# Performance work log

Hardware: AMD Instinct MI355X
Metric: run time of the kernel (lower is better)

## Reference

```python
import jax, jax.numpy as jnp
import numpy as np

# --- module hyperparameters (init_kwargs) ---
K = 64
PZ, PY, PX = 5, 5, 5          # patch_size
PROJ = 512                     # projection_dim
B, C, D, H, W = 4, 256, 32, 64, 64


def setup_inputs() -> dict:
    key = jax.random.key(0)
    k1, k2, k3, k4 = jax.random.split(key, 4)
    feature_map = jax.random.normal(k1, (B, C, D, H, W), jnp.float32)
    score_map = jax.random.normal(k2, (B, 1, D, H, W), jnp.float32)
    # LazyLinear(projection_dim) materialized: in_features = C * K
    Wp = jax.random.normal(k3, (PROJ, C * K), jnp.float32) / np.sqrt(C * K).astype(np.float32)
    b = jax.random.normal(k4, (PROJ,), jnp.float32) * 0.01
    return {"feature_map": feature_map, "score_map": score_map, "Wp": Wp, "b": b}


def reference(feature_map, score_map, Wp, b):
    Bn, Cn, Dn, Hn, Wn = feature_map.shape
    flat = score_map.reshape(Bn, -1)                      # (B, D*H*W)
    scores, idx = jax.lax.top_k(flat, K)                  # (B, K)
    z = idx // (Hn * Wn)
    y = (idx % (Hn * Wn)) // Wn
    x = idx % Wn
    centers = jnp.stack([z, y, x], axis=-1)               # (B, K, 3)

    # boundary-clamped window origins: z0 = max(cz - dz//2, 0), window [z0, min(z0+dz, D))
    z0 = jnp.maximum(z - PZ // 2, 0)
    y0 = jnp.maximum(y - PY // 2, 0)
    x0 = jnp.maximum(x - PX // 2, 0)

    def per_batch(fm, z0b, y0b, x0b):
        # fm: (C, D, H, W); z0b/y0b/x0b: (K,)
        iz = z0b[:, None] + jnp.arange(PZ)                # (K, PZ)
        iy = y0b[:, None] + jnp.arange(PY)
        ix = x0b[:, None] + jnp.arange(PX)
        mz, my, mx = iz < Dn, iy < Hn, ix < Wn            # out-of-range => excluded from mean
        iz = jnp.minimum(iz, Dn - 1)
        iy = jnp.minimum(iy, Hn - 1)
        ix = jnp.minimum(ix, Wn - 1)
        # gather fixed-size patches: (C, K, PZ, PY, PX)
        patch = fm[:, iz[:, :, None, None], iy[:, None, :, None], ix[:, None, None, :]]
        mask = (mz[:, :, None, None] & my[:, None, :, None] & mx[:, None, None, :]).astype(fm.dtype)  # (K,PZ,PY,PX)
        s = jnp.einsum('ckzyx,kzyx->kc', patch, mask)     # masked sum -> (K, C)
        cnt = mask.sum(axis=(-3, -2, -1))                 # (K,) = actual clamped patch volume
        return (s / cnt[:, None]).reshape(-1)             # (K*C,) — patch-major, matching torch cat order

    vec = jax.vmap(per_batch)(feature_map, z0, y0, x0)    # (B, K*C)
    feature = vec @ Wp.T + b                              # (B, PROJ)
    return centers, scores, feature
```

## Files before the change

### kernel.cpp

```cpp
#include <hip/hip_runtime.h>
#include <hip/hip_bf16.h>

#define Bn   4
#define Cn   256
#define Dn   32
#define Hn   64
#define Wn   64
#define Kt   64
#define PROJ 512
#define DHW  (Dn*Hn*Wn)
#define HW   (Hn*Wn)
#define VECLEN (Kt*Cn)

#define NBIN    4096
#define CANDMAX 4096
#define STATIC_THR 3.0f

#define WS_CNT_OFF  0
#define WS_IDX_OFF  1024
#define WS_CAND_OFF 4096
#define WS_VEC_OFF  (256*1024)

#define OUT_SCORES 768
#define OUT_FEAT   1024

__device__ __forceinline__ unsigned f2sortable(float f) {
    unsigned u = __float_as_uint(f);
    return (u & 0x80000000u) ? ~u : (u | 0x80000000u);
}
__device__ __forceinline__ float sortable2f(unsigned u) {
    unsigned orig = (u & 0x80000000u) ? (u & 0x7FFFFFFFu) : ~u;
    return __uint_as_float(orig);
}

__global__ __launch_bounds__(256) void compact_kernel(
        const float* __restrict__ score, unsigned long long* __restrict__ cand,
        int* __restrict__ cnt) {
    const int blk = blockIdx.x;
    const int b   = blk >> 6;
    const int sub = blk & 63;
    const int tid = threadIdx.x;
    const unsigned thr = f2sortable(STATIC_THR);

    const float4* src = (const float4*)(score + (size_t)b * DHW) + sub * 512;
    unsigned long long* cb = cand + (size_t)b * CANDMAX;
    #pragma unroll
    for (int i = tid; i < 512; i += 256) {
        float4 v = src[i];
        unsigned gbase = (unsigned)((sub * 512 + i) * 4);
        float vals[4] = {v.x, v.y, v.z, v.w};
        #pragma unroll
        for (int l = 0; l < 4; ++l) {
            unsigned u = f2sortable(vals[l]);
            if (u >= thr) {
                int pos = atomicAdd(&cnt[b], 1);
                if (pos < CANDMAX)
                    cb[pos] = ((unsigned long long)u << 32) |
                              (0xFFFFFFFFu - (gbase + l));
            }
        }
    }
}

__global__ __launch_bounds__(512) void final_kernel(
        const float* __restrict__ score,
        const unsigned long long* __restrict__ cand, const int* __restrict__ cnt,
        float* __restrict__ out, int* __restrict__ topk_idx) {
    __shared__ unsigned long long keys[CANDMAX];
    __shared__ int lh[NBIN];
    __shared__ int partial[256];
    __shared__ int s_cnt, s_thr;
    const int b   = blockIdx.x;
    const int tid = threadIdx.x;

    int n = cnt[b];
    if (n >= Kt && n <= CANDMAX) {
        const unsigned long long* cb = cand + (size_t)b * CANDMAX;
        for (int i = tid; i < n; i += 512) keys[i] = cb[i];
    } else {
        for (int i = tid; i < NBIN; i += 512) lh[i] = 0;
        if (tid == 0) s_cnt = 0;
        __syncthreads();
        const float4* src = (const float4*)(score + (size_t)b * DHW);
        for (int i = tid; i < DHW / 4; i += 512) {
            float4 v = src[i];
            atomicAdd(&lh[f2sortable(v.x) >> 20], 1);
            atomicAdd(&lh[f2sortable(v.y) >> 20], 1);
            atomicAdd(&lh[f2sortable(v.z) >> 20], 1);
            atomicAdd(&lh[f2sortable(v.w) >> 20], 1);
        }
        __syncthreads();
        if (tid < 256) {
            int base = NBIN - 16 - 16 * tid;
            int s = 0;
            #pragma unroll
            for (int i = 0; i < 16; ++i) s += lh[base + i];
            partial[tid] = s;
        }
        __syncthreads();
        if (tid == 0) {
            int cum = 0, T = 0;
            for (int j = 0; j < 256; ++j) {
                if (cum + partial[j] >= Kt) {
                    int bb = NBIN - 1 - 16 * j;
                    for (int i = 0; i < 16; ++i) {
                        cum += lh[bb - i];
                        if (cum >= Kt) { T = bb - i; break; }
                    }
                    break;
                }
                cum += partial[j];
            }
            s_thr = T;
        }
        __syncthreads();
        const unsigned thr = (unsigned)s_thr;
        for (int i = tid; i < DHW / 4; i += 512) {
            float4 v = src[i];
            float vals[4] = {v.x, v.y, v.z, v.w};
            #pragma unroll
            for (int l = 0; l < 4; ++l) {
                unsigned u = f2sortable(vals[l]);
                if ((u >> 20) >= thr) {
                    int pos = atomicAdd(&s_cnt, 1);
                    if (pos < CANDMAX)
                        keys[pos] = ((unsigned long long)u << 32) |
                                    (0xFFFFFFFFu - (unsigned)(4 * i + l));
                }
            }
        }
        __syncthreads();
        n = s_cnt;
        if (n > CANDMAX) n = CANDMAX;
    }

    int P = 64;
    while (P < n) P <<= 1;
    for (int i = tid; i < P; i += 512)
        if (i >= n) keys[i] = 0ULL;
    __syncthreads();

    for (int k = 2; k <= P; k <<= 1) {
        for (int j = k >> 1; j > 0; j >>= 1) {
            for (int i = tid; i < P; i += 512) {
                int ixj = i ^ j;
                if (ixj > i) {
                    unsigned long long a = keys[i], c = keys[ixj];
                    bool desc = ((i & k) == 0);
                    if (desc ? (a < c) : (a > c)) { keys[i] = c; keys[ixj] = a; }
                }
            }
            __syncthreads();
        }
    }

    if (tid < Kt) {
        unsigned long long kk = keys[tid];
        float sc = sortable2f((unsigned)(kk >> 32));
        unsigned gidx = 0xFFFFFFFFu - (unsigned)(kk & 0xFFFFFFFFu);
        int z = (int)(gidx >> 12);
        int y = (int)((gidx >> 6) & 63);
        int x = (int)(gidx & 63);
        int o = (b * Kt + tid) * 3;
        out[o + 0] = (float)z;
        out[o + 1] = (float)y;
        out[o + 2] = (float)x;
        out[OUT_SCORES + b * Kt + tid] = sc;
        topk_idx[b * Kt + tid] = (int)gidx;
    }
}

__global__ __launch_bounds__(256) void gather_kernel(
        const float* __restrict__ fm, const int* __restrict__ topk_idx,
        float* __restrict__ vec) {
    const int blk = blockIdx.x;
    const int b   = blk >> 6;
    const int cg  = blk & 63;
    const int tid = threadIdx.x;
    const int k   = tid & 63;
    const int c   = cg * 4 + (tid >> 6);

    const int idx = topk_idx[b * Kt + k];
    const int z = idx >> 12;
    const int y = (idx >> 6) & 63;
    const int x = idx & 63;
    const int z0 = max(z - 2, 0), y0 = max(y - 2, 0), x0 = max(x - 2, 0);
    const int nz = min(5, Dn - z0), ny = min(5, Hn - y0), nx = min(5, Wn - x0);
    const int xe = x0 + nx;
    const int a0 = x0 & ~3;
    const bool need2 = (a0 + 4) < xe;

    float m[8];
    #pragma unroll
    for (int j = 0; j < 8; ++j) {
        int e = a0 + j;
        m[j] = (e >= x0 && e < xe) ? 1.f : 0.f;
    }

    const float* base = fm + ((size_t)(b * Cn + c)) * DHW
                           + (size_t)z0 * HW + (size_t)y0 * Wn;
    float s = 0.f;
    #pragma unroll
    for (int iz = 0; iz < 5; ++iz) {
        #pragma unroll
        for (int iy = 0; iy < 5; ++iy) {
            if (iz < nz && iy < ny) {
                const float* row = base + iz * HW + iy * Wn;
                float4 v0 = *(const float4*)(row + a0);
                s = fmaf(v0.x, m[0], s);
                s = fmaf(v0.y, m[1], s);
                s = fmaf(v0.z, m[2], s);
                s = fmaf(v0.w, m[3], s);
                if (need2) {
                    float4 v1 = *(const float4*)(row + a0 + 4);
                    s = fmaf(v1.x, m[4], s);
                    s = fmaf(v1.y, m[5], s);
                    s = fmaf(v1.z, m[6], s);
                    s = fmaf(v1.w, m[7], s);
                }
            }
        }
    }
    vec[((size_t)(b * Kt + k) << 8) + c] = s / (float)(nz * ny * nx);
}

__global__ __launch_bounds__(256) void gemv_kernel(
        const float* __restrict__ vec, const float* __restrict__ Wp,
        const float* __restrict__ bias, float* __restrict__ out) {
    const int p   = blockIdx.x;
    const int tid = threadIdx.x;
    const float4* w4 = (const float4*)(Wp + (size_t)p * VECLEN);

    float acc[Bn] = {0.f, 0.f, 0.f, 0.f};
    for (int i = tid; i < VECLEN / 4; i += 256) {
        float4 wv = w4[i];
        #pragma unroll
        for (int bb = 0; bb < Bn; ++bb) {
            float4 vv = ((const float4*)(vec + bb * VECLEN))[i];
            acc[bb] += wv.x * vv.x + wv.y * vv.y + wv.z * vv.z + wv.w * vv.w;
        }
    }

    __shared__ float red[4][Bn];
    const int lane = tid & 63, wave = tid >> 6;
    #pragma unroll
    for (int bb = 0; bb < Bn; ++bb) {
        float v = acc[bb];
        #pragma unroll
        for (int off = 32; off > 0; off >>= 1) v += __shfl_down(v, off, 64);
        if (lane == 0) red[wave][bb] = v;
    }
    __syncthreads();
    if (tid < Bn) {
        int bb = tid;
        float t = red[0][bb] + red[1][bb] + red[2][bb] + red[3][bb];
        out[OUT_FEAT + bb * PROJ + p] = t + bias[p];
    }
}

extern "C" void kernel_launch(void* const* d_in, const int* in_sizes, int n_in,
                              void* d_out, int out_size, void* d_ws, size_t ws_size,
                              hipStream_t stream) {
    const float* fm    = (const float*)d_in[0];
    const float* score = (const float*)d_in[1];
    const float* Wp    = (const float*)d_in[2];
    const float* bias  = (const float*)d_in[3];
    float* out = (float*)d_out;

    char* ws = (char*)d_ws;
    int*   cand_cnt = (int*)(ws + WS_CNT_OFF);
    int*   topk_idx = (int*)(ws + WS_IDX_OFF);
    unsigned long long* cand = (unsigned long long*)(ws + WS_CAND_OFF);
    float* vec      = (float*)(ws + WS_VEC_OFF);

    hipMemsetAsync(cand_cnt, 0, Bn * sizeof(int), stream);
    compact_kernel<<<Bn * 64, 256, 0, stream>>>(score, cand, cand_cnt);
    final_kernel<<<Bn, 512, 0, stream>>>(score, cand, cand_cnt, out, topk_idx);
    gather_kernel<<<Bn * 64, 256, 0, stream>>>(fm, topk_idx, vec);
    gemv_kernel<<<PROJ, 256, 0, stream>>>(vec, Wp, bias, out);
}
```

Before: 71.00 us.

## Use per-block candidate slots and rank-based top-k selection instead of bitonic sort

Compaction now gathers candidates in shared memory per block and writes them to a fixed per-block slot with a count header. This removes the global atomics and the memset launch. The final kernel prefix-sums the slot counts, gathers the keys, and picks the top-K by counting ranks with an O(n^2) comparison instead of a full bitonic sort, now using 256 threads. The risk is the quadratic rank cost if the candidate count is large, plus a fallback path whenever any slot overflows.

```diff
diff --git a/kernel.cpp b/kernel.cpp
--- a/kernel.cpp
+++ b/kernel.cpp
@@ -14,12 +14,12 @@
 
 #define NBIN    4096
 #define CANDMAX 4096
+#define SLOT    128
 #define STATIC_THR 3.0f
 
-#define WS_CNT_OFF  0
-#define WS_IDX_OFF  1024
-#define WS_CAND_OFF 4096
-#define WS_VEC_OFF  (256*1024)
+#define WS_CAND_OFF 0
+#define WS_IDX_OFF  (256*1024)
+#define WS_VEC_OFF  (260*1024)
 
 #define OUT_SCORES 768
 #define OUT_FEAT   1024
@@ -34,16 +34,18 @@
 }
 
 __global__ __launch_bounds__(256) void compact_kernel(
-        const float* __restrict__ score, unsigned long long* __restrict__ cand,
-        int* __restrict__ cnt) {
+        const float* __restrict__ score, unsigned long long* __restrict__ cand) {
+    __shared__ unsigned long long lc[SLOT - 1];
+    __shared__ int lcnt;
     const int blk = blockIdx.x;
     const int b   = blk >> 6;
     const int sub = blk & 63;
     const int tid = threadIdx.x;
+    if (tid == 0) lcnt = 0;
+    __syncthreads();
+
     const unsigned thr = f2sortable(STATIC_THR);
-
     const float4* src = (const float4*)(score + (size_t)b * DHW) + sub * 512;
-    unsigned long long* cb = cand + (size_t)b * CANDMAX;
     #pragma unroll
     for (int i = tid; i < 512; i += 256) {
         float4 v = src[i];
@@ -53,36 +55,65 @@
         for (int l = 0; l < 4; ++l) {
             unsigned u = f2sortable(vals[l]);
             if (u >= thr) {
-                int pos = atomicAdd(&cnt[b], 1);
-                if (pos < CANDMAX)
-                    cb[pos] = ((unsigned long long)u << 32) |
+                int pos = atomicAdd(&lcnt, 1);
+                if (pos < SLOT - 1)
+                    lc[pos] = ((unsigned long long)u << 32) |
                               (0xFFFFFFFFu - (gbase + l));
             }
         }
     }
-}
-
-__global__ __launch_bounds__(512) void final_kernel(
+    __syncthreads();
+
+    unsigned long long* cb = cand + (size_t)blk * SLOT;
+    int n = lcnt;
+    if (n > SLOT - 1) n = SLOT;
+    if (tid == 0) cb[0] = (unsigned long long)n;
+    int m = (n > SLOT - 1) ? (SLOT - 1) : n;
+    for (int i = tid; i < m; i += 256) cb[1 + i] = lc[i];
+}
+
+__global__ __launch_bounds__(256) void final_kernel(
         const float* __restrict__ score,
-        const unsigned long long* __restrict__ cand, const int* __restrict__ cnt,
+        const unsigned long long* __restrict__ cand,
         float* __restrict__ out, int* __restrict__ topk_idx) {
     __shared__ unsigned long long keys[CANDMAX];
+    __shared__ unsigned long long win[Kt];
     __shared__ int lh[NBIN];
     __shared__ int partial[256];
-    __shared__ int s_cnt, s_thr;
+    __shared__ int cnts[64], offs[64];
+    __shared__ int s_n, s_thr, s_cnt, s_ovf;
     const int b   = blockIdx.x;
     const int tid = threadIdx.x;
 
-    int n = cnt[b];
-    if (n >= Kt && n <= CANDMAX) {
-        const unsigned long long* cb = cand + (size_t)b * CANDMAX;
-        for (int i = tid; i < n; i += 512) keys[i] = cb[i];
+    if (tid == 0) { s_ovf = 0; s_cnt = 0; }
+    __syncthreads();
+    if (tid < 64) {
+        int c = (int)cand[(size_t)((b << 6) + tid) * SLOT];
+        if (c > SLOT - 1) atomicOr(&s_ovf, 1);
+        cnts[tid] = c;
+    }
+    __syncthreads();
+    if (tid == 0) {
+        int o = 0;
+        for (int s = 0; s < 64; ++s) { offs[s] = o; o += cnts[s]; }
+        s_n = o;
+    }
+    __syncthreads();
+
+    int n = s_n;
+    if (!s_ovf && n >= Kt && n <= CANDMAX) {
+        for (int s = 0; s < 64; ++s) {
+            int c = cnts[s], o = offs[s];
+            const unsigned long long* cb =
+                cand + (size_t)((b << 6) + s) * SLOT + 1;
+            for (int i = tid; i < c; i += 256) keys[o + i] = cb[i];
+        }
+        __syncthreads();
     } else {
-        for (int i = tid; i < NBIN; i += 512) lh[i] = 0;
-        if (tid == 0) s_cnt = 0;
+        for (int i = tid; i < NBIN; i += 256) lh[i] = 0;
         __syncthreads();
         const float4* src = (const float4*)(score + (size_t)b * DHW);
-        for (int i = tid; i < DHW / 4; i += 512) {
+        for (int i = tid; i < DHW / 4; i += 256) {
             float4 v = src[i];
             atomicAdd(&lh[f2sortable(v.x) >> 20], 1);
             atomicAdd(&lh[f2sortable(v.y) >> 20], 1);
@@ -90,7 +121,7 @@
             atomicAdd(&lh[f2sortable(v.w) >> 20], 1);
         }
         __syncthreads();
-        if (tid < 256) {
+        {
             int base = NBIN - 16 - 16 * tid;
             int s = 0;
             #pragma unroll
@@ -115,7 +146,7 @@
         }
         __syncthreads();
         const unsigned thr = (unsigned)s_thr;
-        for (int i = tid; i < DHW / 4; i += 512) {
+        for (int i = tid; i < DHW / 4; i += 256) {
             float4 v = src[i];
             float vals[4] = {v.x, v.y, v.z, v.w};
             #pragma unroll
@@ -134,28 +165,16 @@
         if (n > CANDMAX) n = CANDMAX;
     }
 
-    int P = 64;
-    while (P < n) P <<= 1;
-    for (int i = tid; i < P; i += 512)
-        if (i >= n) keys[i] = 0ULL;
-    __syncthreads();
-
-    for (int k = 2; k <= P; k <<= 1) {
-        for (int j = k >> 1; j > 0; j >>= 1) {
-            for (int i = tid; i < P; i += 512) {
-                int ixj = i ^ j;
-                if (ixj > i) {
-                    unsigned long long a = keys[i], c = keys[ixj];
-                    bool desc = ((i & k) == 0);
-                    if (desc ? (a < c) : (a > c)) { keys[i] = c; keys[ixj] = a; }
-                }
-            }
-            __syncthreads();
-        }
-    }
+    for (int i = tid; i < n; i += 256) {
+        unsigned long long k = keys[i];
+        int r = 0;
+        for (int j = 0; j < n; ++j) r += (keys[j] > k);
+        if (r < Kt) win[r] = k;
+    }
+    __syncthreads();
 
     if (tid < Kt) {
-        unsigned long long kk = keys[tid];
+        unsigned long long kk = win[tid];
         float sc = sortable2f((unsigned)(kk >> 32));
         unsigned gidx = 0xFFFFFFFFu - (unsigned)(kk & 0xFFFFFFFFu);
         int z = (int)(gidx >> 12);
@@ -268,14 +287,12 @@
     float* out = (float*)d_out;
 
     char* ws = (char*)d_ws;
-    int*   cand_cnt = (int*)(ws + WS_CNT_OFF);
+    unsigned long long* cand = (unsigned long long*)(ws + WS_CAND_OFF);
     int*   topk_idx = (int*)(ws + WS_IDX_OFF);
-    unsigned long long* cand = (unsigned long long*)(ws + WS_CAND_OFF);
     float* vec      = (float*)(ws + WS_VEC_OFF);
 
-    hipMemsetAsync(cand_cnt, 0, Bn * sizeof(int), stream);
-    compact_kernel<<<Bn * 64, 256, 0, stream>>>(score, cand, cand_cnt);
-    final_kernel<<<Bn, 512, 0, stream>>>(score, cand, cand_cnt, out, topk_idx);
+    compact_kernel<<<Bn * 64, 256, 0, stream>>>(score, cand);
+    final_kernel<<<Bn, 256, 0, stream>>>(score, cand, out, topk_idx);
     gather_kernel<<<Bn * 64, 256, 0, stream>>>(fm, topk_idx, vec);
     gemv_kernel<<<PROJ, 256, 0, stream>>>(vec, Wp, bias, out);
 }
```

After: 66.20 us. 6.8% less time.
